# Kernel tuning notes

Hardware: AMD Instinct MI355X
Metric: run time of the kernel (lower is better)

Reference implementation:

```python
import jax, jax.numpy as jnp
import numpy as np

EPS = 1e-16
N = 1024
DEG = 8
NUM_COMB = 6      # comb(DEG-2, DEG-3)
NUM_COMB_I = 21   # comb(DEG-1, 2)


def _gather_rows(vals, idx):
    # vals: (N, N); idx: (N, ...) -> out[i, ...] = vals[i, idx[i, ...]]
    return jax.vmap(lambda v, i: v[i])(vals, idx)


def setup_inputs() -> dict:
    key = jax.random.key(0)
    ks = jax.random.split(key, 17)
    f = jnp.float32
    return {
        "X": jax.random.uniform(ks[0], (N, N), f),
        "T": jnp.ones((1,), f),
        "C": jax.random.uniform(ks[1], (N, N, 1), f),
        "D": jax.random.uniform(ks[2], (N, N, 1), f),
        "S": jax.random.uniform(ks[3], (N, N, 1), f),
        "mask": jax.random.uniform(ks[4], (N, N, 1), f),
        "b0": jax.random.uniform(ks[5], (1,), f),
        "b1": jax.random.uniform(ks[6], (1,), f),
        "b2": jax.random.uniform(ks[7], (1,), f),
        "lam": jax.random.uniform(ks[8], (1,), f),
        "eta": jax.random.uniform(ks[9], (1,), f),
        "nu": jax.random.uniform(ks[10], (1,), f),
        "mu": jax.random.uniform(ks[11], (1,), f),
        "kap": jax.random.uniform(ks[12], (1, DEG - 2), f),
        "idx_ij": jax.random.randint(ks[13], (N, N, DEG - 2, 1), 0, N),
        "idx_ijF": jax.random.randint(ks[14], (N, N, NUM_COMB, 1), 0, N),
        "idx_ijT": jax.random.randint(ks[15], (N, N, NUM_COMB, DEG - 3, 1), 0, N),
        "idx_iT": jax.random.randint(ks[16], (N, NUM_COMB_I, 2, 1), 0, N),
        "b": 0,
    }


def reference(X, T, C, D, S, mask, b0, b1, b2, lam, eta, nu, mu, kap,
              idx_ij, idx_ijF, idx_ijT, idx_iT, b):
    t = T[0]
    ij = idx_ij[..., b]          # (N, N, DEG-2)
    ijF = idx_ijF[..., b]        # (N, N, NUM_COMB)
    ijT = idx_ijT[..., b]        # (N, N, NUM_COMB, DEG-3)
    iT = idx_iT[..., b]          # (N, NUM_COMB_I, 2)
    Cb, Db, Sb, mb = C[..., b], D[..., b], S[..., b], mask[..., b]

    X_ = 1.0 - X + EPS
    XT = X.T
    lX_ = jnp.log(X_)
    row_lsum = jnp.sum(lX_, axis=1)            # (N,)
    tmp0 = jnp.exp(row_lsum[:, None] - lX_)    # (N, N)
    XX_ = X / X_

    g_ij = _gather_rows(XX_, ij)               # (N, N, DEG-2)
    locUp0 = jnp.sum(g_ij, axis=2)
    g_ijF = _gather_rows(XX_, ijF)             # (N, N, NUM_COMB)
    g_ijT = _gather_rows(XX_, ijT)             # (N, N, NUM_COMB, DEG-3)
    locUp1 = jnp.sum(g_ijF * jnp.sum(g_ijT, axis=3), axis=2)

    pair = lam + eta * Db + nu * Cb + mu * Sb  # (N, N)
    gX_ij = _gather_rows(X, ij)                # (N, N, DEG-2)

    gamma = (b1 - b0 + (b2 - b1) * locUp0 - b2 * locUp1) * tmp0
    gamma = gamma + (4.0 * XT - 2.0) * pair + 100.0 * (mb - 1.0) \
            + jnp.sum((4.0 * gX_ij - 2.0) * kap[0], axis=2)

    g_iT = _gather_rows(XX_, iT)               # (N, NUM_COMB_I, 2)
    elb = b0[0] + jnp.sum(XX_, axis=1) * b1[0] \
          + jnp.sum(jnp.prod(g_iT, axis=2), axis=1) * b2[0]    # (N,)
    elb = jnp.sum(elb * jnp.exp(row_lsum))
    elb = elb + jnp.sum(pair * (1.0 + 4.0 * X * XT - 2.0 * (X + XT)) * mb)
    # X3D[:, :DEG-2, :].transpose(1,2)[i,k,m] == X[i,k] broadcast over m
    Xk = X[:, :, None]
    term3 = (1.0 - 2.0 * (gX_ij + Xk) + 4.0 * (gX_ij * Xk)) * kap[0]
    elb = elb + jnp.sum(jnp.sum(term3, axis=2) * mb)
    elb = elb - t * jnp.sum((X * jnp.log(X + EPS) + X_ * lX_) * mb)

    return elb, jax.nn.sigmoid(gamma / t)
```

## Files before the change

### kernel.cpp

```cpp
#include <hip/hip_runtime.h>

#define NN 1024
#define EPSF 1e-16f

__device__ __forceinline__ float wave_red(float v){
  #pragma unroll
  for(int o=32;o>0;o>>=1) v += __shfl_down(v, o, 64);
  return v;
}

__global__ void transpose_k(const float* __restrict__ in, float* __restrict__ out){
  __shared__ float tile[32][33];
  int bx=blockIdx.x*32, by=blockIdx.y*32;
  int tx=threadIdx.x, ty=threadIdx.y;
  #pragma unroll
  for(int r=0;r<32;r+=8) tile[ty+r][tx] = in[(by+ty+r)*NN + bx+tx];
  __syncthreads();
  #pragma unroll
  for(int r=0;r<32;r+=8) out[(bx+ty+r)*NN + by+tx] = tile[tx][ty+r];
}

__global__ __launch_bounds__(256) void main_k(
    const float* __restrict__ X,  const float* __restrict__ XT,
    const float* __restrict__ C,  const float* __restrict__ D,
    const float* __restrict__ S,  const float* __restrict__ M,
    const float* __restrict__ Tp, const float* __restrict__ b0p,
    const float* __restrict__ b1p,const float* __restrict__ b2p,
    const float* __restrict__ lamp,const float* __restrict__ etap,
    const float* __restrict__ nup, const float* __restrict__ mup,
    const float* __restrict__ kapp,
    const int* __restrict__ idx_ij, const int* __restrict__ idx_ijF,
    const int* __restrict__ idx_ijT,const int* __restrict__ idx_iT,
    float* __restrict__ out, double* __restrict__ elb_acc)
{
  __shared__ float s_x[NN], s_xx[NN], s_lx[NN];
  __shared__ float red0[4], red1[4];
  __shared__ float s_bc[1];
  const int i = blockIdx.x, tid = threadIdx.x;

  const float tv  = Tp[0];
  const float b0v = b0p[0], b1v = b1p[0], b2v = b2p[0];
  const float lamv= lamp[0], etav= etap[0], nuv = nup[0], muv = mup[0];
  float kapv[6];
  #pragma unroll
  for(int k=0;k<6;k++) kapv[k]=kapp[k];

  float4 xv = ((const float4*)(X + (size_t)i*NN))[tid];
  float lsum=0.f, xsum=0.f;
  #pragma unroll
  for(int s=0;s<4;s++){
    float x  = (&xv.x)[s];
    float x_ = 1.0f - x + EPSF;
    float lx = logf(x_);
    float xx = x / x_;
    int jj = tid*4+s;
    s_x[jj]=x; s_xx[jj]=xx; s_lx[jj]=lx;
    lsum += lx; xsum += xx;
  }
  float wl = wave_red(lsum), wx = wave_red(xsum);
  if((tid&63)==0){ red0[tid>>6]=wl; red1[tid>>6]=wx; }
  __syncthreads();
  if(tid==0){
    float rl = red0[0]+red0[1]+red0[2]+red0[3];
    float rx = red1[0]+red1[1]+red1[2]+red1[3];
    s_bc[0]=rl;
    float sp=0.f;
    const int* pit = idx_iT + (size_t)i*42;
    for(int c=0;c<21;c++) sp += s_xx[pit[2*c]] * s_xx[pit[2*c+1]];
    float er = (b0v + rx*b1v + sp*b2v) * expf(rl);
    atomicAdd(elb_acc, (double)er);
  }
  __syncthreads();
  const float rowlsum = s_bc[0];
  const float inv_t = 1.0f / tv;

  float acc = 0.f;
  #pragma unroll 1
  for(int q=0;q<4;q++){
    int j = q*256 + tid;
    size_t base = (size_t)i*NN + j;
    float x  = s_x[j];
    float lx = s_lx[j];
    float x_ = 1.0f - x + EPSF;
    float tmp0 = expf(rowlsum - lx);
    float xt = XT[base];
    float cb = C[base], db = D[base], sb = S[base], mb = M[base];
    float pair = lamv + etav*db + nuv*cb + muv*sb;

    const int* pij = idx_ij + base*6;
    float locUp0=0.f, kapsum=0.f, t3=0.f;
    #pragma unroll
    for(int k=0;k<6;k++){
      int a = pij[k];
      float gx = s_x[a];
      locUp0 += s_xx[a];
      kapsum += (4.f*gx - 2.f)*kapv[k];
      t3     += (1.f - 2.f*(gx + x) + 4.f*gx*x)*kapv[k];
    }
    const int* pf = idx_ijF + base*6;
    const int* pt = idx_ijT + base*30;
    float locUp1=0.f;
    #pragma unroll
    for(int c=0;c<6;c++){
      float s=0.f;
      #pragma unroll
      for(int d=0;d<5;d++) s += s_xx[pt[c*5+d]];
      locUp1 += s_xx[pf[c]]*s;
    }
    float gamma = (b1v - b0v + (b2v-b1v)*locUp0 - b2v*locUp1)*tmp0
                + (4.f*xt - 2.f)*pair + 100.f*(mb - 1.f) + kapsum;
    out[1 + base] = 1.0f/(1.0f + expf(-gamma*inv_t));

    float e = pair*(1.f + 4.f*x*xt - 2.f*(x + xt))*mb
            + t3*mb
            - tv*(x*logf(x + EPSF) + x_*lx)*mb;
    acc += e;
  }
  float wa = wave_red(acc);
  if((tid&63)==0) red0[tid>>6]=wa;
  __syncthreads();
  if(tid==0){
    double tot = (double)red0[0] + (double)red0[1] + (double)red0[2] + (double)red0[3];
    atomicAdd(elb_acc, tot);
  }
}

__global__ void finalize_k(const double* __restrict__ acc, float* __restrict__ out){
  if(threadIdx.x==0) out[0] = (float)(*acc);
}

extern "C" void kernel_launch(void* const* d_in, const int* in_sizes, int n_in,
                              void* d_out, int out_size, void* d_ws, size_t ws_size,
                              hipStream_t stream){
  const float* X   = (const float*)d_in[0];
  const float* T   = (const float*)d_in[1];
  const float* C   = (const float*)d_in[2];
  const float* D   = (const float*)d_in[3];
  const float* S   = (const float*)d_in[4];
  const float* M   = (const float*)d_in[5];
  const float* b0  = (const float*)d_in[6];
  const float* b1  = (const float*)d_in[7];
  const float* b2  = (const float*)d_in[8];
  const float* lam = (const float*)d_in[9];
  const float* eta = (const float*)d_in[10];
  const float* nu  = (const float*)d_in[11];
  const float* mu  = (const float*)d_in[12];
  const float* kap = (const float*)d_in[13];
  const int* iij   = (const int*)d_in[14];
  const int* iijF  = (const int*)d_in[15];
  const int* iijT  = (const int*)d_in[16];
  const int* iiT   = (const int*)d_in[17];
  float* out = (float*)d_out;

  double* elb_acc = (double*)d_ws;
  float*  XT = (float*)((char*)d_ws + 16);

  hipMemsetAsync(d_ws, 0, 8, stream);
  transpose_k<<<dim3(32,32), dim3(32,8), 0, stream>>>(X, XT);
  main_k<<<dim3(1024), dim3(256), 0, stream>>>(X, XT, C, D, S, M,
      T, b0, b1, b2, lam, eta, nu, mu, kap,
      iij, iijF, iijT, iiT, out, elb_acc);
  finalize_k<<<1, 64, 0, stream>>>(elb_acc, out);
}
```

Before: 282.7 us.

## Split each row across four blocks and vectorize index loads

Each row is now handled by four blocks, each covering 256 columns, instead of one block looping over four chunks. Every block recomputes the row's log-sum prologue in shared memory, and only chunk 0 adds the per-row elb term. The index arrays are read as int2 vectors into registers before the gathers, which gives more memory-level parallelism and more blocks in flight. The cost is four times the prologue work and more atomics on the accumulator.

```diff
diff --git a/kernel.cpp b/kernel.cpp
--- a/kernel.cpp
+++ b/kernel.cpp
@@ -36,7 +36,10 @@
   __shared__ float s_x[NN], s_xx[NN], s_lx[NN];
   __shared__ float red0[4], red1[4];
   __shared__ float s_bc[1];
-  const int i = blockIdx.x, tid = threadIdx.x;
+  const int bid = blockIdx.x;
+  const int i = bid >> 2;
+  const int chunk = bid & 3;
+  const int tid = threadIdx.x;
 
   const float tv  = Tp[0];
   const float b0v = b0p[0], b1v = b1p[0], b2v = b2p[0];
@@ -62,61 +65,74 @@
   __syncthreads();
   if(tid==0){
     float rl = red0[0]+red0[1]+red0[2]+red0[3];
-    float rx = red1[0]+red1[1]+red1[2]+red1[3];
     s_bc[0]=rl;
-    float sp=0.f;
-    const int* pit = idx_iT + (size_t)i*42;
-    for(int c=0;c<21;c++) sp += s_xx[pit[2*c]] * s_xx[pit[2*c+1]];
-    float er = (b0v + rx*b1v + sp*b2v) * expf(rl);
-    atomicAdd(elb_acc, (double)er);
+    if(chunk==0){
+      float rx = red1[0]+red1[1]+red1[2]+red1[3];
+      float sp=0.f;
+      const int* pit = idx_iT + (size_t)i*42;
+      for(int c=0;c<21;c++) sp += s_xx[pit[2*c]] * s_xx[pit[2*c+1]];
+      float er = (b0v + rx*b1v + sp*b2v) * expf(rl);
+      atomicAdd(elb_acc, (double)er);
+    }
   }
   __syncthreads();
   const float rowlsum = s_bc[0];
   const float inv_t = 1.0f / tv;
 
-  float acc = 0.f;
-  #pragma unroll 1
-  for(int q=0;q<4;q++){
-    int j = q*256 + tid;
-    size_t base = (size_t)i*NN + j;
-    float x  = s_x[j];
-    float lx = s_lx[j];
-    float x_ = 1.0f - x + EPSF;
-    float tmp0 = expf(rowlsum - lx);
-    float xt = XT[base];
-    float cb = C[base], db = D[base], sb = S[base], mb = M[base];
-    float pair = lamv + etav*db + nuv*cb + muv*sb;
+  const int j = chunk*256 + tid;
+  const size_t base = (size_t)i*NN + j;
 
-    const int* pij = idx_ij + base*6;
-    float locUp0=0.f, kapsum=0.f, t3=0.f;
+  int idxA[6], idxF[6], idxT[30];
+  {
+    const int2* p = (const int2*)(idx_ij + base*6);
     #pragma unroll
-    for(int k=0;k<6;k++){
-      int a = pij[k];
-      float gx = s_x[a];
-      locUp0 += s_xx[a];
-      kapsum += (4.f*gx - 2.f)*kapv[k];
-      t3     += (1.f - 2.f*(gx + x) + 4.f*gx*x)*kapv[k];
-    }
-    const int* pf = idx_ijF + base*6;
-    const int* pt = idx_ijT + base*30;
-    float locUp1=0.f;
+    for(int k=0;k<3;k++){ int2 v=p[k]; idxA[2*k]=v.x; idxA[2*k+1]=v.y; }
+  }
+  {
+    const int2* p = (const int2*)(idx_ijF + base*6);
     #pragma unroll
-    for(int c=0;c<6;c++){
-      float s=0.f;
-      #pragma unroll
-      for(int d=0;d<5;d++) s += s_xx[pt[c*5+d]];
-      locUp1 += s_xx[pf[c]]*s;
-    }
-    float gamma = (b1v - b0v + (b2v-b1v)*locUp0 - b2v*locUp1)*tmp0
-                + (4.f*xt - 2.f)*pair + 100.f*(mb - 1.f) + kapsum;
-    out[1 + base] = 1.0f/(1.0f + expf(-gamma*inv_t));
+    for(int k=0;k<3;k++){ int2 v=p[k]; idxF[2*k]=v.x; idxF[2*k+1]=v.y; }
+  }
+  {
+    const int2* p = (const int2*)(idx_ijT + base*30);
+    #pragma unroll
+    for(int k=0;k<15;k++){ int2 v=p[k]; idxT[2*k]=v.x; idxT[2*k+1]=v.y; }
+  }
+  float xt = XT[base];
+  float cb = C[base], db = D[base], sb = S[base], mb = M[base];
 
-    float e = pair*(1.f + 4.f*x*xt - 2.f*(x + xt))*mb
-            + t3*mb
-            - tv*(x*logf(x + EPSF) + x_*lx)*mb;
-    acc += e;
+  float x  = s_x[j];
+  float lx = s_lx[j];
+  float x_ = 1.0f - x + EPSF;
+  float tmp0 = expf(rowlsum - lx);
+  float pair = lamv + etav*db + nuv*cb + muv*sb;
+
+  float locUp0=0.f, kapsum=0.f, t3=0.f;
+  #pragma unroll
+  for(int k=0;k<6;k++){
+    int a = idxA[k];
+    float gx = s_x[a];
+    locUp0 += s_xx[a];
+    kapsum += (4.f*gx - 2.f)*kapv[k];
+    t3     += (1.f - 2.f*(gx + x) + 4.f*gx*x)*kapv[k];
   }
-  float wa = wave_red(acc);
+  float locUp1=0.f;
+  #pragma unroll
+  for(int c=0;c<6;c++){
+    float s=0.f;
+    #pragma unroll
+    for(int d=0;d<5;d++) s += s_xx[idxT[c*5+d]];
+    locUp1 += s_xx[idxF[c]]*s;
+  }
+  float gamma = (b1v - b0v + (b2v-b1v)*locUp0 - b2v*locUp1)*tmp0
+              + (4.f*xt - 2.f)*pair + 100.f*(mb - 1.f) + kapsum;
+  out[1 + base] = 1.0f/(1.0f + expf(-gamma*inv_t));
+
+  float e = pair*(1.f + 4.f*x*xt - 2.f*(x + xt))*mb
+          + t3*mb
+          - tv*(x*logf(x + EPSF) + x_*lx)*mb;
+
+  float wa = wave_red(e);
   if((tid&63)==0) red0[tid>>6]=wa;
   __syncthreads();
   if(tid==0){
@@ -157,7 +173,7 @@
 
   hipMemsetAsync(d_ws, 0, 8, stream);
   transpose_k<<<dim3(32,32), dim3(32,8), 0, stream>>>(X, XT);
-  main_k<<<dim3(1024), dim3(256), 0, stream>>>(X, XT, C, D, S, M,
+  main_k<<<dim3(4096), dim3(256), 0, stream>>>(X, XT, C, D, S, M,
       T, b0, b1, b2, lam, eta, nu, mu, kap,
       iij, iijF, iijT, iiT, out, elb_acc);
   finalize_k<<<1, 64, 0, stream>>>(elb_acc, out);
```

Result: no change. 282.4 us (-0.1%).
